# Optimization experiments

Hardware: AMD Instinct MI355X
Metric: run time of the kernel (lower is better)

## Reference

```python
import jax, jax.numpy as jnp
import numpy as np

# ---- dims (match init_kwargs) ----
P = 512          # num_prototypes
NB = 16          # num_blocks
D = 2048         # d_model
DB = D // NB     # d_block = 128
TEMP = 1.0
B, N = 8, 4096
EPS = 1e-5


def block_ln(x):
    """LayerNorm over each d_block chunk, no affine (BlockLayerNorm)."""
    lead = x.shape[:-1]
    xb = x.reshape(*lead, NB, DB)
    mu = jnp.mean(xb, axis=-1, keepdims=True)
    var = jnp.mean(jnp.square(xb - mu), axis=-1, keepdims=True)
    xb = (xb - mu) * jax.lax.rsqrt(var + EPS)
    return xb.reshape(*lead, NB * DB)


def setup_inputs() -> dict:
    key = jax.random.key(0)
    ks = jax.random.split(key, 10)
    h = 4 * DB

    def lin(k, fan_out, fan_in):
        # xavier-ish init for the custom linear()
        s = (2.0 / (fan_in + fan_out)) ** 0.5
        return jax.random.normal(k, (fan_out, fan_in), jnp.float32) * s

    return {
        "queries": jax.random.normal(ks[0], (B, N, D), jnp.float32),
        "mem_params": jax.random.truncated_normal(ks[1], -2.0, 2.0, (1, P, NB, DB), jnp.float32),
        "w1": lin(ks[2], h, DB),  "b1": jnp.zeros((h,), jnp.float32),
        "w2": lin(ks[3], h, h),   "b2": jnp.zeros((h,), jnp.float32),
        "w3": lin(ks[4], h, h),   "b3": jnp.zeros((h,), jnp.float32),
        "w4": lin(ks[5], DB, h),  "b4": jnp.zeros((DB,), jnp.float32),
    }


def reference(queries, mem_params, w1, b1, w2, b2, w3, b3, w4, b4):
    # mem_proj: per-block 4-layer MLP on mem_params [1, P, NB, DB]
    h = jax.nn.relu(mem_params @ w1.T + b1)
    h = jax.nn.relu(h @ w2.T + b2)
    h = jax.nn.relu(h @ w3.T + b3)
    mem = h @ w4.T + b4                                  # [1, P, NB, DB]

    mem = block_ln(mem.reshape(1, P, D))                 # norm_mem
    q = block_ln(queries)                                # norm_query

    # BlockAttention: per-block attention over prototypes
    qb = q.reshape(B, N, NB, DB) * (DB ** -0.5)          # [B, N, NB, DB]
    kvb = mem.reshape(1, P, NB, DB)                      # [1, P, NB, DB] (k == v)

    scores = jnp.einsum('bnhd,zmhd->bhnm', qb, kvb) / TEMP   # [B, NB, N, P]
    attn = jax.nn.softmax(scores, axis=-1)
    out = jnp.einsum('bhnm,zmhd->bnhd', attn, kvb)           # [B, N, NB, DB]
    return out.reshape(B, N, D)
```

## Files before the change

### kernel.cpp

```cpp
#include <hip/hip_runtime.h>

#define P_   512
#define NB_  16
#define D_   2048
#define DB_  128
#define H_   512
#define B_   8
#define N_   4096

typedef __attribute__((ext_vector_type(8))) short short8;
typedef __attribute__((ext_vector_type(4))) float f32x4;

static __device__ __forceinline__ short f2bf(float x) {
    union { float f; unsigned u; } v; v.f = x;
    unsigned r = (v.u + 0x7FFF + ((v.u >> 16) & 1)) >> 16;
    return (short)r;
}

__global__ __launch_bounds__(256) void k_convert(
    const float* __restrict__ memp, const float* __restrict__ w1,
    const float* __restrict__ w2, const float* __restrict__ w3,
    const float* __restrict__ w4, short* __restrict__ dst)
{
    const int total = 1048576 + 65536 + 262144 + 262144 + 65536;
    for (int i = blockIdx.x * 256 + threadIdx.x; i < total; i += gridDim.x * 256) {
        int j = i; float v;
        if (j < 1048576) v = memp[j];
        else {
            j -= 1048576;
            if (j < 65536) v = w1[j];
            else { j -= 65536;
                if (j < 262144) v = w2[j];
                else { j -= 262144;
                    if (j < 262144) v = w3[j];
                    else v = w4[j - 262144];
                }
            }
        }
        dst[i] = f2bf(v);
    }
}

template<int BM, int BN, int K, int MODE>
__global__ __launch_bounds__(256) void k_gemm(
    const short* __restrict__ A, const short* __restrict__ Bw,
    const float* __restrict__ bias, short* __restrict__ Out, int Nn)
{
    constexpr int MT = BM / 64;
    constexpr int NT = BN / 16;
    __shared__ short As[BM * 72];
    __shared__ short Bs[BN * 72];

    const int tid = threadIdx.x;
    const int w = tid >> 6, l = tid & 63;
    const int lr = l & 15, lq = l >> 4;
    const int nblk = (MODE == 1) ? 1 : (512 / BN);
    const int m0 = (blockIdx.x / nblk) * BM;
    const int n0 = (blockIdx.x % nblk) * BN;

    f32x4 acc[MT][NT] = {};

    for (int k0 = 0; k0 < K; k0 += 64) {
        #pragma unroll
        for (int i = tid * 8; i < BM * 64; i += 2048) {
            int r = i >> 6, c = i & 63;
            *(short8*)&As[r * 72 + c] = *(const short8*)&A[(size_t)(m0 + r) * K + k0 + c];
        }
        #pragma unroll
        for (int i = tid * 8; i < BN * 64; i += 2048) {
            int r = i >> 6, c = i & 63;
            *(short8*)&Bs[r * 72 + c] = *(const short8*)&Bw[(size_t)(n0 + r) * K + k0 + c];
        }
        __syncthreads();
        #pragma unroll
        for (int ks = 0; ks < 2; ++ks) {
            short8 bf[NT];
            #pragma unroll
            for (int nt = 0; nt < NT; ++nt)
                bf[nt] = *(const short8*)&Bs[(nt * 16 + lr) * 72 + ks * 32 + lq * 8];
            #pragma unroll
            for (int mt = 0; mt < MT; ++mt) {
                short8 af = *(const short8*)&As[((w * MT + mt) * 16 + lr) * 72 + ks * 32 + lq * 8];
                #pragma unroll
                for (int nt = 0; nt < NT; ++nt)
                    acc[mt][nt] = __builtin_amdgcn_mfma_f32_16x16x32_bf16(af, bf[nt], acc[mt][nt], 0, 0, 0);
            }
        }
        __syncthreads();
    }

    if (MODE == 0) {
        #pragma unroll
        for (int mt = 0; mt < MT; ++mt) {
            #pragma unroll
            for (int nt = 0; nt < NT; ++nt) {
                float bv = bias[n0 + nt * 16 + lr];
                #pragma unroll
                for (int r = 0; r < 4; ++r) {
                    int row = m0 + (w * MT + mt) * 16 + lq * 4 + r;
                    float v = acc[mt][nt][r] + bv;
                    v = fmaxf(v, 0.f);
                    Out[(size_t)row * Nn + n0 + nt * 16 + lr] = f2bf(v);
                }
            }
        }
    } else {
        float vals[NT][4];
        float sum[4] = {0,0,0,0}, sq[4] = {0,0,0,0};
        #pragma unroll
        for (int nt = 0; nt < NT; ++nt) {
            float bv = bias[nt * 16 + lr];
            #pragma unroll
            for (int r = 0; r < 4; ++r) {
                float v = acc[0][nt][r] + bv;
                vals[nt][r] = v; sum[r] += v; sq[r] += v * v;
            }
        }
        #pragma unroll
        for (int m = 1; m < 16; m <<= 1) {
            #pragma unroll
            for (int r = 0; r < 4; ++r) {
                sum[r] += __shfl_xor(sum[r], m);
                sq[r]  += __shfl_xor(sq[r], m);
            }
        }
        #pragma unroll
        for (int r = 0; r < 4; ++r) {
            float mu = sum[r] * (1.f / 128.f);
            float var = sq[r] * (1.f / 128.f) - mu * mu;
            float rstd = rsqrtf(var + 1e-5f);
            int vrow = m0 + w * 16 + lq * 4 + r;
            int nb = vrow & 15, p = vrow >> 4;
            #pragma unroll
            for (int nt = 0; nt < NT; ++nt)
                Out[((size_t)(nb * 512 + p)) * 128 + nt * 16 + lr] = f2bf((vals[nt][r] - mu) * rstd);
        }
    }
}

__global__ __launch_bounds__(256) void k_transpose(const short* __restrict__ mem, short* __restrict__ memT)
{
    int bid = blockIdx.x;
    int nb = bid >> 4, pt = (bid >> 1) & 7, dt = bid & 1;
    __shared__ short t[64 * 72];
    const short* src = mem + ((size_t)(nb * 512 + pt * 64)) * 128 + dt * 64;
    for (int i = threadIdx.x * 8; i < 64 * 64; i += 2048) {
        int p = i >> 6, d = i & 63;
        *(short8*)&t[p * 72 + d] = *(const short8*)&src[(size_t)p * 128 + d];
    }
    __syncthreads();
    short* dst = memT + ((size_t)(nb * 128 + dt * 64)) * 512 + pt * 64;
    for (int i = threadIdx.x * 8; i < 64 * 64; i += 2048) {
        int d = i >> 6, p = i & 63;
        short8 v;
        #pragma unroll
        for (int j = 0; j < 8; ++j) v[j] = t[(p + j) * 72 + d];
        *(short8*)&dst[(size_t)d * 512 + p] = v;
    }
}

__global__ __launch_bounds__(256, 2) void k_attn(
    const float* __restrict__ q, const short* __restrict__ mem,
    const short* __restrict__ memT, float* __restrict__ out)
{
    alignas(16) __shared__ char smem[54272];
    short* qs  = (short*)smem;
    short* ktb = (short*)smem;
    short* vtb = (short*)(smem + 17408);
    short* pb  = (short*)(smem + 35840);

    const int x = blockIdx.x;
    const int qt = x & 31, h = (x >> 5) & 15, b = x >> 9;
    const int tid = threadIdx.x, w = tid >> 6, l = tid & 63;
    const int q0 = qt * 128;
    const int lr = l & 15, lq = l >> 4;

    const float* qbase = q + ((size_t)(b * N_ + q0)) * D_ + h * DB_;
    #pragma unroll
    for (int g = 0; g < 4; ++g) {
        int row = w * 32 + g * 8 + (l >> 3);
        int c0 = (l & 7) * 16;
        const float* rp = qbase + (size_t)row * D_ + c0;
        float x16[16];
        float s = 0.f, sq2 = 0.f;
        #pragma unroll
        for (int u = 0; u < 16; u += 4) {
            f32x4 v4 = *(const f32x4*)(rp + u);
            #pragma unroll
            for (int j = 0; j < 4; ++j) { float v = v4[j]; x16[u + j] = v; s += v; sq2 += v * v; }
        }
        s += __shfl_xor(s, 1);  sq2 += __shfl_xor(sq2, 1);
        s += __shfl_xor(s, 2);  sq2 += __shfl_xor(sq2, 2);
        s += __shfl_xor(s, 4);  sq2 += __shfl_xor(sq2, 4);
        float mu = s * (1.f / 128.f);
        float var = sq2 * (1.f / 128.f) - mu * mu;
        float rstd = rsqrtf(var + 1e-5f) * 0.08838834764831845f;
        short tmp[16];
        #pragma unroll
        for (int u = 0; u < 16; ++u) tmp[u] = f2bf((x16[u] - mu) * rstd);
        *(short8*)&qs[row * 136 + c0]     = *(short8*)&tmp[0];
        *(short8*)&qs[row * 136 + c0 + 8] = *(short8*)&tmp[8];
    }
    short8 qf[2][4];
    #pragma unroll
    for (int mt = 0; mt < 2; ++mt)
        #pragma unroll
        for (int ks = 0; ks < 4; ++ks)
            qf[mt][ks] = *(const short8*)&qs[(w * 32 + mt * 16 + lr) * 136 + ks * 32 + lq * 8];
    __syncthreads();

    f32x4 o[2][8] = {};
    float rs[2][4] = {};
    const short* memh  = mem  + (size_t)h * 512 * 128;
    const short* memTh = memT + (size_t)h * 128 * 512;

    for (int kt = 0; kt < 8; ++kt) {
        #pragma unroll
        for (int i = tid * 8; i < 64 * 128; i += 2048) {
            int p = i >> 7, d = i & 127;
            *(short8*)&ktb[p * 136 + d] = *(const short8*)&memh[(size_t)(kt * 64 + p) * 128 + d];
        }
        #pragma unroll
        for (int i = tid * 8; i < 128 * 64; i += 2048) {
            int d = i >> 6, p = i & 63;
            *(short8*)&vtb[d * 72 + p] = *(const short8*)&memTh[(size_t)d * 512 + kt * 64 + p];
        }
        __syncthreads();

        #pragma unroll
        for (int mt = 0; mt < 2; ++mt) {
            #pragma unroll
            for (int nt = 0; nt < 4; ++nt) {
                f32x4 s = {};
                #pragma unroll
                for (int ks = 0; ks < 4; ++ks) {
                    short8 bf = *(const short8*)&ktb[(nt * 16 + lr) * 136 + ks * 32 + lq * 8];
                    s = __builtin_amdgcn_mfma_f32_16x16x32_bf16(qf[mt][ks], bf, s, 0, 0, 0);
                }
                #pragma unroll
                for (int r = 0; r < 4; ++r) {
                    float e = __expf(s[r]);
                    rs[mt][r] += e;
                    pb[(w * 32 + mt * 16 + lq * 4 + r) * 72 + nt * 16 + lr] = f2bf(e);
                }
            }
        }
        short8 af[2][2];
        #pragma unroll
        for (int mt = 0; mt < 2; ++mt)
            #pragma unroll
            for (int k2 = 0; k2 < 2; ++k2)
                af[mt][k2] = *(const short8*)&pb[(w * 32 + mt * 16 + lr) * 72 + k2 * 32 + lq * 8];
        #pragma unroll
        for (int ntd = 0; ntd < 8; ++ntd) {
            #pragma unroll
            for (int k2 = 0; k2 < 2; ++k2) {
                short8 bf = *(const short8*)&vtb[(ntd * 16 + lr) * 72 + k2 * 32 + lq * 8];
                #pragma unroll
                for (int mt = 0; mt < 2; ++mt)
                    o[mt][ntd] = __builtin_amdgcn_mfma_f32_16x16x32_bf16(af[mt][k2], bf, o[mt][ntd], 0, 0, 0);
            }
        }
        __syncthreads();
    }

    #pragma unroll
    for (int mt = 0; mt < 2; ++mt)
        #pragma unroll
        for (int r = 0; r < 4; ++r) {
            float v = rs[mt][r];
            v += __shfl_xor(v, 1); v += __shfl_xor(v, 2);
            v += __shfl_xor(v, 4); v += __shfl_xor(v, 8);
            rs[mt][r] = 1.f / v;
        }
    float* ob = out + ((size_t)(b * N_ + q0)) * D_ + h * DB_;
    #pragma unroll
    for (int mt = 0; mt < 2; ++mt)
        #pragma unroll
        for (int ntd = 0; ntd < 8; ++ntd)
            #pragma unroll
            for (int r = 0; r < 4; ++r)
                ob[(size_t)(w * 32 + mt * 16 + lq * 4 + r) * D_ + ntd * 16 + lr] = o[mt][ntd][r] * rs[mt][r];
}

extern "C" void kernel_launch(void* const* d_in, const int* in_sizes, int n_in,
                              void* d_out, int out_size, void* d_ws, size_t ws_size,
                              hipStream_t stream) {
    const float* queries = (const float*)d_in[0];
    const float* memp    = (const float*)d_in[1];
    const float* w1 = (const float*)d_in[2]; const float* b1 = (const float*)d_in[3];
    const float* w2 = (const float*)d_in[4]; const float* b2 = (const float*)d_in[5];
    const float* w3 = (const float*)d_in[6]; const float* b3 = (const float*)d_in[7];
    const float* w4 = (const float*)d_in[8]; const float* b4 = (const float*)d_in[9];
    float* out = (float*)d_out;

    short* ws      = (short*)d_ws;
    short* memp_b  = ws;
    short* w1b     = memp_b + 1048576;
    short* w2b     = w1b + 65536;
    short* w3b     = w2b + 262144;
    short* w4b     = w3b + 262144;
    short* act1    = w4b + 65536;
    short* act2    = act1 + 4194304;
    short* memb    = act2 + 4194304;
    short* memTb   = memb + 1048576;

    k_convert<<<2048, 256, 0, stream>>>(memp, w1, w2, w3, w4, ws);
    k_gemm<128, 64, 128, 0><<<512, 256, 0, stream>>>(memp_b, w1b, b1, act1, 512);
    k_gemm<128, 64, 512, 0><<<512, 256, 0, stream>>>(act1, w2b, b2, act2, 512);
    k_gemm<128, 64, 512, 0><<<512, 256, 0, stream>>>(act2, w3b, b3, act1, 512);
    k_gemm<64, 128, 512, 1><<<128, 256, 0, stream>>>(act1, w4b, b4, memb, 128);
    k_transpose<<<256, 256, 0, stream>>>(memb, memTb);
    k_attn<<<4096, 256, 0, stream>>>(queries, memb, memTb, out);
}
```

Baseline: 786.8 us.

## Read K/V directly from global memory in attention, drop LDS staging and barriers

The attention kernel no longer stages K and V tiles through shared memory with block-wide barriers. Each wave now loads MFMA B-fragments straight from global or L2 memory, keeps per-wave private LDS regions for Q and the probability tile, and raises the occupancy hint to 3 blocks per CU. Separately, the MLP GEMMs use 128x128 tiles with half the grid. The aim is to remove barrier stalls and LDS traffic and to raise occupancy, at the cost of more redundant global/L2 loads per wave and less latency hiding for those loads.

```diff
diff --git a/kernel.cpp b/kernel.cpp
--- a/kernel.cpp
+++ b/kernel.cpp
@@ -159,15 +159,12 @@
     }
 }
 
-__global__ __launch_bounds__(256, 2) void k_attn(
+__global__ __launch_bounds__(256, 3) void k_attn(
     const float* __restrict__ q, const short* __restrict__ mem,
     const short* __restrict__ memT, float* __restrict__ out)
 {
-    alignas(16) __shared__ char smem[54272];
-    short* qs  = (short*)smem;
-    short* ktb = (short*)smem;
-    short* vtb = (short*)(smem + 17408);
-    short* pb  = (short*)(smem + 35840);
+    __shared__ short qs[4 * 32 * 136];
+    __shared__ short pb[4 * 32 * 72];
 
     const int x = blockIdx.x;
     const int qt = x & 31, h = (x >> 5) & 15, b = x >> 9;
@@ -175,12 +172,15 @@
     const int q0 = qt * 128;
     const int lr = l & 15, lq = l >> 4;
 
+    short* qsw = qs + w * (32 * 136);
+    short* pbw = pb + w * (32 * 72);
+
     const float* qbase = q + ((size_t)(b * N_ + q0)) * D_ + h * DB_;
     #pragma unroll
     for (int g = 0; g < 4; ++g) {
-        int row = w * 32 + g * 8 + (l >> 3);
+        int lrow = g * 8 + (l >> 3);
         int c0 = (l & 7) * 16;
-        const float* rp = qbase + (size_t)row * D_ + c0;
+        const float* rp = qbase + (size_t)(w * 32 + lrow) * D_ + c0;
         float x16[16];
         float s = 0.f, sq2 = 0.f;
         #pragma unroll
@@ -198,16 +198,9 @@
         short tmp[16];
         #pragma unroll
         for (int u = 0; u < 16; ++u) tmp[u] = f2bf((x16[u] - mu) * rstd);
-        *(short8*)&qs[row * 136 + c0]     = *(short8*)&tmp[0];
-        *(short8*)&qs[row * 136 + c0 + 8] = *(short8*)&tmp[8];
-    }
-    short8 qf[2][4];
-    #pragma unroll
-    for (int mt = 0; mt < 2; ++mt)
-        #pragma unroll
-        for (int ks = 0; ks < 4; ++ks)
-            qf[mt][ks] = *(const short8*)&qs[(w * 32 + mt * 16 + lr) * 136 + ks * 32 + lq * 8];
-    __syncthreads();
+        *(short8*)&qsw[lrow * 136 + c0]     = *(short8*)&tmp[0];
+        *(short8*)&qsw[lrow * 136 + c0 + 8] = *(short8*)&tmp[8];
+    }
 
     f32x4 o[2][8] = {};
     float rs[2][4] = {};
@@ -215,53 +208,48 @@
     const short* memTh = memT + (size_t)h * 128 * 512;
 
     for (int kt = 0; kt < 8; ++kt) {
-        #pragma unroll
-        for (int i = tid * 8; i < 64 * 128; i += 2048) {
-            int p = i >> 7, d = i & 127;
-            *(short8*)&ktb[p * 136 + d] = *(const short8*)&memh[(size_t)(kt * 64 + p) * 128 + d];
-        }
-        #pragma unroll
-        for (int i = tid * 8; i < 128 * 64; i += 2048) {
-            int d = i >> 6, p = i & 63;
-            *(short8*)&vtb[d * 72 + p] = *(const short8*)&memTh[(size_t)d * 512 + kt * 64 + p];
-        }
-        __syncthreads();
-
-        #pragma unroll
-        for (int mt = 0; mt < 2; ++mt) {
-            #pragma unroll
-            for (int nt = 0; nt < 4; ++nt) {
-                f32x4 s = {};
-                #pragma unroll
-                for (int ks = 0; ks < 4; ++ks) {
-                    short8 bf = *(const short8*)&ktb[(nt * 16 + lr) * 136 + ks * 32 + lq * 8];
-                    s = __builtin_amdgcn_mfma_f32_16x16x32_bf16(qf[mt][ks], bf, s, 0, 0, 0);
-                }
-                #pragma unroll
-                for (int r = 0; r < 4; ++r) {
-                    float e = __expf(s[r]);
-                    rs[mt][r] += e;
-                    pb[(w * 32 + mt * 16 + lq * 4 + r) * 72 + nt * 16 + lr] = f2bf(e);
-                }
-            }
-        }
+        short8 qf[2][4];
+        #pragma unroll
+        for (int mt = 0; mt < 2; ++mt)
+            #pragma unroll
+            for (int ks = 0; ks < 4; ++ks)
+                qf[mt][ks] = *(const short8*)&qsw[(mt * 16 + lr) * 136 + ks * 32 + lq * 8];
+
+        #pragma unroll
+        for (int nt = 0; nt < 4; ++nt) {
+            f32x4 s0 = {}, s1 = {};
+            #pragma unroll
+            for (int ks = 0; ks < 4; ++ks) {
+                short8 bf = *(const short8*)&memh[(size_t)(kt * 64 + nt * 16 + lr) * 128 + ks * 32 + lq * 8];
+                s0 = __builtin_amdgcn_mfma_f32_16x16x32_bf16(qf[0][ks], bf, s0, 0, 0, 0);
+                s1 = __builtin_amdgcn_mfma_f32_16x16x32_bf16(qf[1][ks], bf, s1, 0, 0, 0);
+            }
+            #pragma unroll
+            for (int r = 0; r < 4; ++r) {
+                float e0 = __expf(s0[r]);
+                float e1 = __expf(s1[r]);
+                rs[0][r] += e0;
+                rs[1][r] += e1;
+                pbw[(lq * 4 + r) * 72 + nt * 16 + lr]        = f2bf(e0);
+                pbw[(16 + lq * 4 + r) * 72 + nt * 16 + lr]   = f2bf(e1);
+            }
+        }
+
         short8 af[2][2];
         #pragma unroll
         for (int mt = 0; mt < 2; ++mt)
             #pragma unroll
             for (int k2 = 0; k2 < 2; ++k2)
-                af[mt][k2] = *(const short8*)&pb[(w * 32 + mt * 16 + lr) * 72 + k2 * 32 + lq * 8];
+                af[mt][k2] = *(const short8*)&pbw[(mt * 16 + lr) * 72 + k2 * 32 + lq * 8];
         #pragma unroll
         for (int ntd = 0; ntd < 8; ++ntd) {
             #pragma unroll
             for (int k2 = 0; k2 < 2; ++k2) {
-                short8 bf = *(const short8*)&vtb[(ntd * 16 + lr) * 72 + k2 * 32 + lq * 8];
-                #pragma unroll
-                for (int mt = 0; mt < 2; ++mt)
-                    o[mt][ntd] = __builtin_amdgcn_mfma_f32_16x16x32_bf16(af[mt][k2], bf, o[mt][ntd], 0, 0, 0);
-            }
-        }
-        __syncthreads();
+                short8 bf = *(const short8*)&memTh[(size_t)(ntd * 16 + lr) * 512 + kt * 64 + k2 * 32 + lq * 8];
+                o[0][ntd] = __builtin_amdgcn_mfma_f32_16x16x32_bf16(af[0][k2], bf, o[0][ntd], 0, 0, 0);
+                o[1][ntd] = __builtin_amdgcn_mfma_f32_16x16x32_bf16(af[1][k2], bf, o[1][ntd], 0, 0, 0);
+            }
+        }
     }
 
     #pragma unroll
@@ -306,9 +294,9 @@
     short* memTb   = memb + 1048576;
 
     k_convert<<<2048, 256, 0, stream>>>(memp, w1, w2, w3, w4, ws);
-    k_gemm<128, 64, 128, 0><<<512, 256, 0, stream>>>(memp_b, w1b, b1, act1, 512);
-    k_gemm<128, 64, 512, 0><<<512, 256, 0, stream>>>(act1, w2b, b2, act2, 512);
-    k_gemm<128, 64, 512, 0><<<512, 256, 0, stream>>>(act2, w3b, b3, act1, 512);
+    k_gemm<128, 128, 128, 0><<<256, 256, 0, stream>>>(memp_b, w1b, b1, act1, 512);
+    k_gemm<128, 128, 512, 0><<<256, 256, 0, stream>>>(act1, w2b, b2, act2, 512);
+    k_gemm<128, 128, 512, 0><<<256, 256, 0, stream>>>(act2, w3b, b3, act1, 512);
     k_gemm<64, 128, 512, 1><<<128, 256, 0, stream>>>(act1, w4b, b4, memb, 128);
     k_transpose<<<256, 256, 0, stream>>>(memb, memTb);
     k_attn<<<4096, 256, 0, stream>>>(queries, memb, memTb, out);
```

Measured after the change: 980.2 us. 24.6% more time.
